# Kernel optimization log

Hardware: AMD Instinct MI355X
Metric: run time of the kernel (lower is better)

## Reference

```python
import jax, jax.numpy as jnp
import numpy as np

TAU = 1.0
K = 10
N_NODES = 1048576
N_GRAPHS = 4096


def setup_inputs() -> dict:
    key = jax.random.key(0)
    k1, k2, k3 = jax.random.split(key, 3)
    # per-node scalar logits
    x = jax.random.normal(k1, (N_NODES, 1), dtype=jnp.float32)
    # uniforms for gumbel noise, kept away from {0,1} for log stability
    uniforms = jax.random.uniform(k2, (N_NODES, 3 * K), dtype=jnp.float32,
                                  minval=1e-6, maxval=1.0 - 1e-6)
    # PyG-style ptr: B+1 cumulative offsets, ptr[0]=0, ptr[-1]=N
    cuts = jnp.sort(jax.random.randint(k3, (N_GRAPHS - 1,), 1, N_NODES))
    ptr = jnp.concatenate([jnp.zeros((1,), cuts.dtype), cuts,
                           jnp.full((1,), N_NODES, cuts.dtype)])
    return {"x": x, "uniforms": uniforms, "ptr": ptr}


def reference(x, uniforms, ptr):
    # x: [N, 1] node logits; uniforms: [N, 3k]; ptr: [B+1] segment offsets
    N = x.shape[0]
    B = ptr.shape[0] - 1
    # node i belongs to graph g where ptr[g] <= i < ptr[g+1]
    seg = jnp.searchsorted(ptr, jnp.arange(N), side="right") - 1  # [N]
    gumbel = -jnp.log(-jnp.log(uniforms))                           # [N, 3k]
    noisy = (gumbel + x) / TAU                                      # [N, 3k]
    # segmented softmax over nodes (dim=0 within each graph), per column
    m = jax.ops.segment_max(noisy, seg, num_segments=B)             # [B, 3k]
    e = jnp.exp(noisy - m[seg])                                     # [N, 3k]
    denom = jax.ops.segment_sum(e, seg, num_segments=B)             # [B, 3k]
    probs = e / denom[seg]                                          # [N, 3k]
    # max over the 3k gumbel samples per node
    samples = jnp.max(probs, axis=1)                                # [N]
    return samples[:, None]                                         # [N, 1]
```

## Files before the change

### kernel.cpp

```cpp
#include <hip/hip_runtime.h>

#define K3 30

__global__ __launch_bounds__(256) void gnn_sample_concrete_kernel(
    const float* __restrict__ x,
    const float* __restrict__ uniforms,
    const int* __restrict__ ptr,
    float* __restrict__ out)
{
    const int g = blockIdx.x;
    const int start = ptr[g];
    const int end = ptr[g + 1];
    const int len = end - start;
    if (len <= 0) return;

    const int tid = threadIdx.x;

    float sacc[K3];
#pragma unroll
    for (int j = 0; j < K3; ++j) sacc[j] = 0.0f;

    const int iters = (len + 255) >> 8;

    for (int it = 0; it < iters; ++it) {
        const int n = start + it * 256 + tid;
        if (n < end) {
            const float xv = x[n];
            const float2* row =
                reinterpret_cast<const float2*>(uniforms + (size_t)n * K3);
#pragma unroll
            for (int k = 0; k < 15; ++k) {
                float2 u = row[k];
                float g0 = -__logf(-__logf(u.x));
                float g1 = -__logf(-__logf(u.y));
                sacc[2 * k]     += __expf(g0 + xv);
                sacc[2 * k + 1] += __expf(g1 + xv);
            }
        }
    }

#pragma unroll
    for (int j = 0; j < K3; ++j) {
        float v = sacc[j];
#pragma unroll
        for (int off = 32; off >= 1; off >>= 1)
            v += __shfl_xor(v, off, 64);
        sacc[j] = v;
    }

    __shared__ float partial[4][K3];
    __shared__ float lsum[K3];
    const int wave = tid >> 6;
    const int lane = tid & 63;
    if (lane == 0) {
#pragma unroll
        for (int j = 0; j < K3; ++j) partial[wave][j] = sacc[j];
    }
    __syncthreads();
    if (tid < K3) {
        float s = partial[0][tid] + partial[1][tid] + partial[2][tid] +
                  partial[3][tid];
        lsum[tid] = __logf(s);
    }
    __syncthreads();

    float ls[K3];
#pragma unroll
    for (int j = 0; j < K3; ++j) ls[j] = lsum[j];

    for (int it = 0; it < iters; ++it) {
        const int n = start + it * 256 + tid;
        if (n < end) {
            const float xv = x[n];
            const float2* row =
                reinterpret_cast<const float2*>(uniforms + (size_t)n * K3);
            float best = -3.0e38f;
#pragma unroll
            for (int k = 0; k < 15; ++k) {
                float2 u = row[k];
                float g0 = -__logf(-__logf(u.x));
                float g1 = -__logf(-__logf(u.y));
                best = fmaxf(best,
                             fmaxf(g0 - ls[2 * k], g1 - ls[2 * k + 1]));
            }
            out[n] = __expf(best + xv);
        }
    }
}

extern "C" void kernel_launch(void* const* d_in, const int* in_sizes, int n_in,
                              void* d_out, int out_size, void* d_ws, size_t ws_size,
                              hipStream_t stream) {
    const float* x        = (const float*)d_in[0];
    const float* uniforms = (const float*)d_in[1];
    const int*   ptr      = (const int*)d_in[2];
    float* out = (float*)d_out;

    const int B = in_sizes[2] - 1;

    gnn_sample_concrete_kernel<<<B, 256, 0, stream>>>(x, uniforms, ptr, out);
}
```

Measured before the change: 87.72 us.

## Assign one wavefront per graph and use base-2 hardware log/exp intrinsics

Each 64-lane wavefront now owns one graph segment, so four graphs share a block. This removes the shared-memory reduction and both block barriers, and the per-column log-sum stays in registers. The transcendentals are rewritten in base-2 form with raw amdgcn log/exp2 builtins and a folded constant offset, which cuts per-element multiplies. Large segments now iterate more times over a single wave, and there is no bounds check on g when B is not a multiple of four.

Result: faster. 80.57 us (-8.1%).

```diff
diff --git a/kernel.cpp b/kernel.cpp
--- a/kernel.cpp
+++ b/kernel.cpp
@@ -1,6 +1,14 @@
 #include <hip/hip_runtime.h>
 
 #define K3 30
+#define KP 15
+
+__device__ __forceinline__ float hw_log2(float a) {
+    return __builtin_amdgcn_logf(a);
+}
+__device__ __forceinline__ float hw_exp2(float a) {
+    return __builtin_amdgcn_exp2f(a);
+}
 
 __global__ __launch_bounds__(256) void gnn_sample_concrete_kernel(
     const float* __restrict__ x,
@@ -8,82 +16,61 @@
     const int* __restrict__ ptr,
     float* __restrict__ out)
 {
-    const int g = blockIdx.x;
+    const int wave = threadIdx.x >> 6;
+    const int lane = threadIdx.x & 63;
+    const int g = (blockIdx.x << 2) + wave;
+
     const int start = ptr[g];
-    const int end = ptr[g + 1];
-    const int len = end - start;
-    if (len <= 0) return;
+    const int end   = ptr[g + 1];
+    if (end <= start) return;
 
-    const int tid = threadIdx.x;
+    float acc[K3];
+#pragma unroll
+    for (int j = 0; j < K3; ++j) acc[j] = 0.0f;
 
-    float sacc[K3];
-#pragma unroll
-    for (int j = 0; j < K3; ++j) sacc[j] = 0.0f;
-
-    const int iters = (len + 255) >> 8;
+    const int iters = (end - start + 63) >> 6;
 
     for (int it = 0; it < iters; ++it) {
-        const int n = start + it * 256 + tid;
+        const int n = start + (it << 6) + lane;
         if (n < end) {
-            const float xv = x[n];
+            const float xe = fmaf(x[n], 1.44269504f, 0.52876637f);
             const float2* row =
                 reinterpret_cast<const float2*>(uniforms + (size_t)n * K3);
 #pragma unroll
-            for (int k = 0; k < 15; ++k) {
+            for (int k = 0; k < KP; ++k) {
                 float2 u = row[k];
-                float g0 = -__logf(-__logf(u.x));
-                float g1 = -__logf(-__logf(u.y));
-                sacc[2 * k]     += __expf(g0 + xv);
-                sacc[2 * k + 1] += __expf(g1 + xv);
+                float t0 = hw_log2(-hw_log2(u.x));
+                float t1 = hw_log2(-hw_log2(u.y));
+                acc[2 * k]     += hw_exp2(xe - t0);
+                acc[2 * k + 1] += hw_exp2(xe - t1);
             }
         }
     }
 
 #pragma unroll
     for (int j = 0; j < K3; ++j) {
-        float v = sacc[j];
+        float v = acc[j];
 #pragma unroll
-        for (int off = 32; off >= 1; off >>= 1)
+        for (int off = 1; off < 64; off <<= 1)
             v += __shfl_xor(v, off, 64);
-        sacc[j] = v;
+        acc[j] = hw_log2(v);
     }
 
-    __shared__ float partial[4][K3];
-    __shared__ float lsum[K3];
-    const int wave = tid >> 6;
-    const int lane = tid & 63;
-    if (lane == 0) {
-#pragma unroll
-        for (int j = 0; j < K3; ++j) partial[wave][j] = sacc[j];
-    }
-    __syncthreads();
-    if (tid < K3) {
-        float s = partial[0][tid] + partial[1][tid] + partial[2][tid] +
-                  partial[3][tid];
-        lsum[tid] = __logf(s);
-    }
-    __syncthreads();
-
-    float ls[K3];
-#pragma unroll
-    for (int j = 0; j < K3; ++j) ls[j] = lsum[j];
-
     for (int it = 0; it < iters; ++it) {
-        const int n = start + it * 256 + tid;
+        const int n = start + (it << 6) + lane;
         if (n < end) {
-            const float xv = x[n];
+            const float xe = fmaf(x[n], 1.44269504f, 0.52876637f);
             const float2* row =
                 reinterpret_cast<const float2*>(uniforms + (size_t)n * K3);
-            float best = -3.0e38f;
+            float mn = 3.0e38f;
 #pragma unroll
-            for (int k = 0; k < 15; ++k) {
+            for (int k = 0; k < KP; ++k) {
                 float2 u = row[k];
-                float g0 = -__logf(-__logf(u.x));
-                float g1 = -__logf(-__logf(u.y));
-                best = fmaxf(best,
-                             fmaxf(g0 - ls[2 * k], g1 - ls[2 * k + 1]));
+                float t0 = hw_log2(-hw_log2(u.x));
+                float t1 = hw_log2(-hw_log2(u.y));
+                mn = fminf(mn, fminf(t0 + acc[2 * k], t1 + acc[2 * k + 1]));
             }
-            out[n] = __expf(best + xv);
+            out[n] = hw_exp2(xe - mn);
         }
     }
 }
@@ -97,6 +84,7 @@
     float* out = (float*)d_out;
 
     const int B = in_sizes[2] - 1;
+    const int blocks = (B + 3) / 4;
 
-    gnn_sample_concrete_kernel<<<B, 256, 0, stream>>>(x, uniforms, ptr, out);
+    gnn_sample_concrete_kernel<<<blocks, 256, 0, stream>>>(x, uniforms, ptr, out);
 }
```
